# Kernel tuning notes

Measured on AMD Instinct MI355X. Metric: run time of the kernel, lower is better.

The kernel has to match this reference:

```python
import jax, jax.numpy as jnp
import numpy as np

N = 50000      # nodes
E = 800000     # edges (before self-loops)
F_IN = 128     # in_dim
H = 8          # heads
C = 16         # out_dim per head
NEG_SLOPE = 0.2
EPS = 1e-5


def setup_inputs() -> dict:
    key = jax.random.key(0)
    ks = jax.random.split(key, 8)
    x = jax.random.normal(ks[0], (N, F_IN), dtype=jnp.float32)
    edge_index = jax.random.randint(ks[1], (2, E), 0, N, dtype=jnp.int64)
    # GAT linear weight (xavier-ish scale), stored as [F_IN, H*C]
    W_gat = jax.random.normal(ks[2], (F_IN, H * C), dtype=jnp.float32) * 0.1
    att_src = jax.random.normal(ks[3], (H, C), dtype=jnp.float32) * 0.1
    att_dst = jax.random.normal(ks[4], (H, C), dtype=jnp.float32) * 0.1
    bias_gat = jnp.zeros((H * C,), dtype=jnp.float32)
    W_skip = jax.random.normal(ks[5], (F_IN, H * C), dtype=jnp.float32) * 0.1
    gamma = jnp.ones((H * C,), dtype=jnp.float32)
    beta = jnp.zeros((H * C,), dtype=jnp.float32)
    return {"x": x, "edge_index": edge_index, "W_gat": W_gat,
            "att_src": att_src, "att_dst": att_dst, "bias_gat": bias_gat,
            "W_skip": W_skip, "gamma": gamma, "beta": beta}


def reference(x, edge_index, W_gat, att_src, att_dst, bias_gat, W_skip, gamma, beta):
    # PyG GATConv default: add self-loops
    loop = jnp.arange(N, dtype=edge_index.dtype)
    src = jnp.concatenate([edge_index[0], loop])  # [E+N]
    dst = jnp.concatenate([edge_index[1], loop])  # [E+N]

    h = (x @ W_gat).reshape(N, H, C)              # [N,H,C]
    a_src = jnp.sum(h * att_src, axis=-1)          # [N,H]
    a_dst = jnp.sum(h * att_dst, axis=-1)          # [N,H]

    e = jax.nn.leaky_relu(a_src[src] + a_dst[dst], NEG_SLOPE)   # [E+N,H]
    # segment softmax over destination nodes
    e_max = jax.ops.segment_max(e, dst, num_segments=N)         # [N,H]
    e_exp = jnp.exp(e - e_max[dst])
    denom = jax.ops.segment_sum(e_exp, dst, num_segments=N)     # [N,H]
    alpha = e_exp / denom[dst]                                   # [E+N,H]

    msg = alpha[:, :, None] * h[src]                             # [E+N,H,C]
    gat_out = jax.ops.segment_sum(msg, dst, num_segments=N)     # [N,H,C]
    gat_out = gat_out.reshape(N, H * C) + bias_gat

    skip_out = x @ W_skip                                        # [N,H*C]
    z = gat_out + 0.1 * skip_out

    mu = jnp.mean(z, axis=-1, keepdims=True)
    var = jnp.mean((z - mu) ** 2, axis=-1, keepdims=True)
    z = (z - mu) * jax.lax.rsqrt(var + EPS) * gamma + beta
    return jax.nn.elu(z)  # dropout is identity in eval mode
```

## Files before the change

kernel.cpp:

```cpp
#include <hip/hip_runtime.h>
#include <hip/hip_bf16.h>

#define N_NODES 50000
#define N_EDGES 800000
#define F_IN    128
#define HC      128
#define NR      8
#define RSZ     6250
#define NCH     16
#define CHSZ    50000
#define NP      50048

typedef __attribute__((ext_vector_type(8))) short bf16x8;
typedef __attribute__((ext_vector_type(4))) float f32x4;

__device__ __forceinline__ float bf2f(unsigned int u16) {
    return __uint_as_float(u16 << 16);
}
__device__ __forceinline__ unsigned int f2bf(float f) {
    unsigned int u = __float_as_uint(f);
    return (u + 0x7fffu + ((u >> 16) & 1u)) >> 16;
}

__global__ __launch_bounds__(256) void k_hist(
    const int* __restrict__ dst,
    const float* __restrict__ Wg, const float* __restrict__ Ws,
    unsigned short* __restrict__ Bfrag, int* __restrict__ part)
{
    const int bid = blockIdx.x;
    const int tid = threadIdx.x;
    if (bid < 128) {
        __shared__ int hist[RSZ];
        const int r = bid & 7, c = bid >> 3;
        const int nb = r * RSZ;
        for (int i = tid; i < RSZ; i += 256) hist[i] = 0;
        __syncthreads();
        const int4* d4 = (const int4*)(dst + c * CHSZ);
        for (int i = tid; i < CHSZ / 4; i += 256) {
            const int4 v = d4[i];
            int b;
            b = v.x - nb; if ((unsigned)b < (unsigned)RSZ) atomicAdd(&hist[b], 1);
            b = v.y - nb; if ((unsigned)b < (unsigned)RSZ) atomicAdd(&hist[b], 1);
            b = v.z - nb; if ((unsigned)b < (unsigned)RSZ) atomicAdd(&hist[b], 1);
            b = v.w - nb; if ((unsigned)b < (unsigned)RSZ) atomicAdd(&hist[b], 1);
        }
        __syncthreads();
        for (int i = tid; i < RSZ; i += 256)
            part[(size_t)c * NP + nb + i] = hist[i];
    } else {
        const int g = (bid - 128) * 256 + tid;
        if (g < 4096) {
            const int lane = g & 63;
            const int kq = (g >> 6) & 3;
            const int nt = g >> 8;
            const int cc = nt * 16 + (lane & 15);
            const int kbase = kq * 32 + (lane >> 4) * 8;
            const float* Wsel = (cc < 128) ? (Wg + cc) : (Ws + cc - 128);
            unsigned int pk[4];
#pragma unroll
            for (int p = 0; p < 4; p++) {
                const float v0 = Wsel[(size_t)(kbase + 2 * p) * HC];
                const float v1 = Wsel[(size_t)(kbase + 2 * p + 1) * HC];
                pk[p] = f2bf(v0) | (f2bf(v1) << 16);
            }
            *(uint4*)(Bfrag + (size_t)g * 8) = make_uint4(pk[0], pk[1], pk[2], pk[3]);
        }
    }
}

__global__ __launch_bounds__(256) void k_scanA(
    int* __restrict__ part, int* __restrict__ counts,
    int* __restrict__ row_start, int* __restrict__ bsum)
{
    __shared__ int s[256];
    const int tid = threadIdx.x;
    const int base = blockIdx.x * 1024 + tid * 4;
    int v[4]; int t = 0;
#pragma unroll
    for (int j = 0; j < 4; j++) {
        const int idx = base + j;
        if (idx < N_NODES) {
            int run = 0;
#pragma unroll
            for (int c = 0; c < 16; c++) {
                int* p = part + (size_t)c * NP + idx;
                const int q = *p;
                *p = run;
                run += q;
            }
            counts[idx] = run;
            v[j] = run + 1;
        } else v[j] = 0;
        t += v[j];
    }
    s[tid] = t;
    __syncthreads();
    for (int off = 1; off < 256; off <<= 1) {
        int add = (tid >= off) ? s[tid - off] : 0;
        __syncthreads();
        s[tid] += add;
        __syncthreads();
    }
    int excl = s[tid] - t;
#pragma unroll
    for (int j = 0; j < 4; j++) {
        const int idx = base + j;
        if (idx < N_NODES) row_start[idx] = excl;
        excl += v[j];
    }
    if (tid == 255) bsum[blockIdx.x] = s[255];
}

__global__ void k_scanB(int* bsum, int nb) {
    int tid = threadIdx.x;
    int v = (tid < nb) ? bsum[tid] : 0;
    int orig = v;
    for (int off = 1; off < 64; off <<= 1) {
        int y = __shfl_up(v, off);
        if (tid >= off) v += y;
    }
    if (tid < nb) bsum[tid] = v - orig;
}

__global__ void k_scanC(int* __restrict__ row_start, const int* __restrict__ bsum,
                        const int* __restrict__ counts, int* __restrict__ csr) {
    int i = blockIdx.x * 256 + threadIdx.x;
    if (i < N_NODES) {
        int rs = row_start[i] + bsum[i >> 10];
        row_start[i] = rs;
        csr[rs + counts[i]] = i;
    }
}

__global__ __launch_bounds__(256) void k_lf(
    const float* __restrict__ x,
    const unsigned short* __restrict__ Bfrag,
    const float* __restrict__ att_s,
    const float* __restrict__ att_d,
    const float* __restrict__ bias,
    unsigned short* __restrict__ h_bf, unsigned int* __restrict__ z0b,
    float* __restrict__ a_src, float* __restrict__ a_dst,
    const int* __restrict__ src, const int* __restrict__ dst,
    const int* __restrict__ row_start, const int* __restrict__ part,
    int* __restrict__ csr)
{
    __shared__ __align__(16) int smem[RSZ];
    const int bid = blockIdx.x;
    const int tid = threadIdx.x;
    int lin = -1, r = 0, c = 0;
    if (bid < 256) {
        const int g = bid >> 4, pos = bid & 15;
        if (pos < 8) { r = pos; c = g; }
        else lin = g * 8 + (pos - 8);
    } else {
        lin = 128 + (bid - 256);
    }

    if (lin < 0) {
        const int nb = r * RSZ;
        for (int b = tid; b < RSZ; b += 256)
            smem[b] = row_start[nb + b] + part[(size_t)c * NP + nb + b];
        __syncthreads();
        const int4* d4 = (const int4*)(dst + c * CHSZ);
        const int4* s4 = (const int4*)(src + c * CHSZ);
        for (int i = tid; i < CHSZ / 4; i += 256) {
            const int4 dv = d4[i];
            const int4 sv = s4[i];
            int b;
            b = dv.x - nb; if ((unsigned)b < (unsigned)RSZ) csr[atomicAdd(&smem[b], 1)] = sv.x;
            b = dv.y - nb; if ((unsigned)b < (unsigned)RSZ) csr[atomicAdd(&smem[b], 1)] = sv.y;
            b = dv.z - nb; if ((unsigned)b < (unsigned)RSZ) csr[atomicAdd(&smem[b], 1)] = sv.z;
            b = dv.w - nb; if ((unsigned)b < (unsigned)RSZ) csr[atomicAdd(&smem[b], 1)] = sv.w;
        }
        return;
    }

    unsigned short* sA = (unsigned short*)smem;
    const int lane = tid & 63;
    const int w = tid >> 6;
    const int nbase = lin * 64;

#pragma unroll
    for (int it = 0; it < 4; it++) {
        const int p = it * 256 + tid;
        const int node = p >> 4;
        const int kg = p & 15;
        const int gn = nbase + node;
        float v[8];
        if (gn < N_NODES) {
            float4 u0 = *(const float4*)(x + (size_t)gn * F_IN + kg * 8);
            float4 u1 = *(const float4*)(x + (size_t)gn * F_IN + kg * 8 + 4);
            v[0] = u0.x; v[1] = u0.y; v[2] = u0.z; v[3] = u0.w;
            v[4] = u1.x; v[5] = u1.y; v[6] = u1.z; v[7] = u1.w;
        } else {
#pragma unroll
            for (int j = 0; j < 8; j++) v[j] = 0.f;
        }
        const int mt = node >> 4, lm = node & 15;
        const int kq = kg >> 2, quad = kg & 3;
        uint4 pk;
        pk.x = f2bf(v[0]) | (f2bf(v[1]) << 16);
        pk.y = f2bf(v[2]) | (f2bf(v[3]) << 16);
        pk.z = f2bf(v[4]) | (f2bf(v[5]) << 16);
        pk.w = f2bf(v[6]) | (f2bf(v[7]) << 16);
        *(uint4*)(sA + ((size_t)((mt * 4 + kq) * 64 + quad * 16 + lm)) * 8) = pk;
    }
    __syncthreads();

    const bf16x8* Bf = (const bf16x8*)Bfrag;
    f32x4 acc[4][4];
#pragma unroll
    for (int mt = 0; mt < 4; mt++)
#pragma unroll
        for (int nt = 0; nt < 4; nt++)
            acc[mt][nt] = (f32x4){0.f, 0.f, 0.f, 0.f};

#pragma unroll
    for (int kq = 0; kq < 4; kq++) {
        bf16x8 aF[4], bF[4];
#pragma unroll
        for (int nt = 0; nt < 4; nt++)
            bF[nt] = Bf[(size_t)(((w * 4 + nt) * 4 + kq) * 64 + lane)];
#pragma unroll
        for (int mt = 0; mt < 4; mt++)
            aF[mt] = *(const bf16x8*)(sA + ((size_t)((mt * 4 + kq) * 64 + lane)) * 8);
#pragma unroll
        for (int mt = 0; mt < 4; mt++)
#pragma unroll
            for (int nt = 0; nt < 4; nt++)
                acc[mt][nt] = __builtin_amdgcn_mfma_f32_16x16x32_bf16(
                    aF[mt], bF[nt], acc[mt][nt], 0, 0, 0);
    }

    const int row4 = (lane >> 4) * 4;
    const int cl = lane & 15;
#pragma unroll
    for (int mt = 0; mt < 4; mt++) {
#pragma unroll
        for (int nt = 0; nt < 4; nt++) {
            const int cc = w * 64 + nt * 16 + cl;
            f32x4 d = acc[mt][nt];
            if (cc < 128) {
                const float asv = att_s[cc];
                const float adv = att_d[cc];
                float ps[4], pd[4];
#pragma unroll
                for (int rr = 0; rr < 4; rr++) { ps[rr] = d[rr] * asv; pd[rr] = d[rr] * adv; }
#pragma unroll
                for (int m = 1; m <= 8; m <<= 1) {
#pragma unroll
                    for (int rr = 0; rr < 4; rr++) {
                        ps[rr] += __shfl_xor(ps[rr], m);
                        pd[rr] += __shfl_xor(pd[rr], m);
                    }
                }
                const int head = w * 4 + nt;
#pragma unroll
                for (int rr = 0; rr < 4; rr++) {
                    const int gn = nbase + mt * 16 + row4 + rr;
                    if (gn < N_NODES) {
                        h_bf[(size_t)gn * HC + cc] = (unsigned short)f2bf(d[rr]);
                        if (cl == 0) {
                            a_src[gn * 8 + head] = ps[rr];
                            a_dst[gn * 8 + head] = pd[rr];
                        }
                    }
                }
            } else {
                const int cz = cc - 128;
                const float bv = bias[cz];
#pragma unroll
                for (int rr = 0; rr < 4; rr++) {
                    const int gn = nbase + mt * 16 + row4 + rr;
                    const float val = 0.1f * d[rr] + bv;
                    const float oth = __shfl_xor(val, 1);
                    if ((cl & 1) == 0 && gn < N_NODES) {
                        z0b[(size_t)gn * 64 + (cz >> 1)] =
                            f2bf(val) | (f2bf(oth) << 16);
                    }
                }
            }
        }
    }
}

__global__ __launch_bounds__(256) void k_agg(
    const uint2* __restrict__ h2,
    const uint2* __restrict__ z0b,
    const float* __restrict__ a_src, const float* __restrict__ a_dst,
    const int* __restrict__ row_start, const int* __restrict__ counts,
    const int* __restrict__ csr,
    const float* __restrict__ gamma, const float* __restrict__ beta,
    float* __restrict__ out)
{
    const int tid = threadIdx.x;
    const int lane = tid & 63;
    const int l = lane & 31;
    const int n = blockIdx.x * 8 + ((tid >> 6) << 1) + (lane >> 5);
    const int head = l >> 2;

    const float adn = a_dst[n * 8 + head];
    const int rs = row_start[n];
    const int cnt = counts[n] + 1;

    float d_acc = 0.f, a0 = 0.f, a1 = 0.f, a2 = 0.f, a3 = 0.f;
    for (int i = 0; i < cnt; i += 8) {
        int s[8]; float ae[8], mk[8]; uint2 hp[8];
#pragma unroll
        for (int j = 0; j < 8; j++) {
            const int e = i + j;
            const int ec = (e < cnt) ? e : (cnt - 1);
            mk[j] = (e < cnt) ? 1.f : 0.f;
            s[j] = csr[rs + ec];
        }
#pragma unroll
        for (int j = 0; j < 8; j++) ae[j] = a_src[s[j] * 8 + head];
#pragma unroll
        for (int j = 0; j < 8; j++) hp[j] = h2[(size_t)s[j] * 32 + l];
#pragma unroll
        for (int j = 0; j < 8; j++) {
            float e = ae[j] + adn;
            e = (e > 0.f) ? e : 0.2f * e;
            const float wgt = __expf(e) * mk[j];
            d_acc += wgt;
            a0 += wgt * bf2f(hp[j].x & 0xffffu);
            a1 += wgt * bf2f(hp[j].x >> 16);
            a2 += wgt * bf2f(hp[j].y & 0xffffu);
            a3 += wgt * bf2f(hp[j].y >> 16);
        }
    }
    const float inv = 1.0f / d_acc;
    const uint2 zp = z0b[(size_t)n * 32 + l];
    float y0 = a0 * inv + bf2f(zp.x & 0xffffu);
    float y1 = a1 * inv + bf2f(zp.x >> 16);
    float y2 = a2 * inv + bf2f(zp.y & 0xffffu);
    float y3 = a3 * inv + bf2f(zp.y >> 16);

    float ss = y0 + y1 + y2 + y3;
#pragma unroll
    for (int off = 1; off < 32; off <<= 1) ss += __shfl_xor(ss, off);
    const float mu = ss * (1.0f / 128.0f);
    const float d0 = y0 - mu, d1 = y1 - mu, d2 = y2 - mu, d3 = y3 - mu;
    float vs = d0 * d0 + d1 * d1 + d2 * d2 + d3 * d3;
#pragma unroll
    for (int off = 1; off < 32; off <<= 1) vs += __shfl_xor(vs, off);
    const float rstd = rsqrtf(vs * (1.0f / 128.0f) + 1e-5f);

    const float4 gv = *(const float4*)(gamma + l * 4);
    const float4 bv = *(const float4*)(beta + l * 4);
    float o0 = d0 * rstd * gv.x + bv.x;
    float o1 = d1 * rstd * gv.y + bv.y;
    float o2 = d2 * rstd * gv.z + bv.z;
    float o3 = d3 * rstd * gv.w + bv.w;
    o0 = (o0 > 0.f) ? o0 : (__expf(o0) - 1.0f);
    o1 = (o1 > 0.f) ? o1 : (__expf(o1) - 1.0f);
    o2 = (o2 > 0.f) ? o2 : (__expf(o2) - 1.0f);
    o3 = (o3 > 0.f) ? o3 : (__expf(o3) - 1.0f);

    *(float4*)(out + (size_t)n * HC + l * 4) = make_float4(o0, o1, o2, o3);
}

extern "C" void kernel_launch(void* const* d_in, const int* in_sizes, int n_in,
                              void* d_out, int out_size, void* d_ws, size_t ws_size,
                              hipStream_t stream) {
    const float* x   = (const float*)d_in[0];
    const int*   ei  = (const int*)d_in[1];
    const float* Wg  = (const float*)d_in[2];
    const float* as_ = (const float*)d_in[3];
    const float* ad_ = (const float*)d_in[4];
    const float* bg  = (const float*)d_in[5];
    const float* Wsk = (const float*)d_in[6];
    const float* gm  = (const float*)d_in[7];
    const float* bt  = (const float*)d_in[8];
    float* out = (float*)d_out;

    char* wsb = (char*)d_ws;
    unsigned short* h_bf  = (unsigned short*)wsb;
    unsigned int*   z0b   = (unsigned int*)(wsb + 12800000);
    float*          a_src = (float*)(wsb + 25600000);
    float*          a_dst = (float*)(wsb + 27200000);
    unsigned short* Bfrag = (unsigned short*)(wsb + 28800000);
    int*   counts = (int*)(wsb + 28865536);
    int*   row_st = (int*)(wsb + 29065728);
    int*   bsum   = (int*)(wsb + 29265920);
    int*   csr    = (int*)(wsb + 29266944);
    int*   part   = (int*)(wsb + 32666944);

    const int* src = ei;
    const int* dst = ei + N_EDGES;

    k_hist <<<144, 256, 0, stream>>>(dst, Wg, Wsk, Bfrag, part);
    k_scanA<<<49, 256, 0, stream>>>(part, counts, row_st, bsum);
    k_scanB<<<1, 64, 0, stream>>>(bsum, 49);
    k_scanC<<<196, 256, 0, stream>>>(row_st, bsum, counts, csr);
    k_lf   <<<910, 256, 0, stream>>>(x, Bfrag, as_, ad_, bg, h_bf, z0b,
                                     a_src, a_dst, src, dst, row_st, part, csr);
    k_agg  <<<N_NODES / 8, 256, 0, stream>>>((const uint2*)h_bf, (const uint2*)z0b,
                                             a_src, a_dst, row_st, counts, csr,
                                             gm, bt, out);
}
```

Measured before the change: 210.4 us.

## Fold block-sum scan into scanC, stage h in LDS, use one wave per node

The separate single-block scan of block sums is removed; each scanC block computes its own prefix offset with a wave reduction, which drops one kernel launch. In k_lf the bf16 h tile is staged through shared memory so it can be written out as coalesced 16-byte stores, and the attention dot products are computed from the staged rows instead of through per-fragment shuffle reductions. k_agg now assigns a full 64-lane wave to each node, with each lane holding two channels instead of four. This gives more parallelism and more in-flight gathers per edge, but issues more instructions per edge and doubles the wave count.

```diff
diff --git a/kernel.cpp b/kernel.cpp
--- a/kernel.cpp
+++ b/kernel.cpp
@@ -111,22 +111,23 @@
     if (tid == 255) bsum[blockIdx.x] = s[255];
 }
 
-__global__ void k_scanB(int* bsum, int nb) {
-    int tid = threadIdx.x;
-    int v = (tid < nb) ? bsum[tid] : 0;
-    int orig = v;
-    for (int off = 1; off < 64; off <<= 1) {
-        int y = __shfl_up(v, off);
-        if (tid >= off) v += y;
-    }
-    if (tid < nb) bsum[tid] = v - orig;
-}
-
-__global__ void k_scanC(int* __restrict__ row_start, const int* __restrict__ bsum,
-                        const int* __restrict__ counts, int* __restrict__ csr) {
-    int i = blockIdx.x * 256 + threadIdx.x;
+__global__ __launch_bounds__(256) void k_scanC(
+    int* __restrict__ row_start, const int* __restrict__ bsum,
+    const int* __restrict__ counts, int* __restrict__ csr)
+{
+    __shared__ int soff;
+    const int tid = threadIdx.x;
+    if (tid < 64) {
+        const int tgt = blockIdx.x >> 2;
+        int v = (tid < 49 && tid < tgt) ? bsum[tid] : 0;
+#pragma unroll
+        for (int off = 1; off < 64; off <<= 1) v += __shfl_xor(v, off);
+        if (tid == 0) soff = v;
+    }
+    __syncthreads();
+    const int i = blockIdx.x * 256 + tid;
     if (i < N_NODES) {
-        int rs = row_start[i] + bsum[i >> 10];
+        const int rs = row_start[i] + soff;
         row_start[i] = rs;
         csr[rs + counts[i]] = i;
     }
@@ -232,61 +233,93 @@
                     aF[mt], bF[nt], acc[mt][nt], 0, 0, 0);
     }
 
+    __syncthreads();
+
     const int row4 = (lane >> 4) * 4;
     const int cl = lane & 15;
-#pragma unroll
-    for (int mt = 0; mt < 4; mt++) {
-#pragma unroll
-        for (int nt = 0; nt < 4; nt++) {
-            const int cc = w * 64 + nt * 16 + cl;
-            f32x4 d = acc[mt][nt];
-            if (cc < 128) {
-                const float asv = att_s[cc];
-                const float adv = att_d[cc];
-                float ps[4], pd[4];
-#pragma unroll
-                for (int rr = 0; rr < 4; rr++) { ps[rr] = d[rr] * asv; pd[rr] = d[rr] * adv; }
-#pragma unroll
-                for (int m = 1; m <= 8; m <<= 1) {
-#pragma unroll
-                    for (int rr = 0; rr < 4; rr++) {
-                        ps[rr] += __shfl_xor(ps[rr], m);
-                        pd[rr] += __shfl_xor(pd[rr], m);
+    unsigned int* hls = (unsigned int*)smem;
+
+    if (w < 2) {
+#pragma unroll
+        for (int mt = 0; mt < 4; mt++) {
+#pragma unroll
+            for (int nt = 0; nt < 4; nt++) {
+                const int cc = w * 64 + nt * 16 + cl;
+                f32x4 d = acc[mt][nt];
+#pragma unroll
+                for (int rr = 0; rr < 4; rr++) {
+                    const float oth = __shfl_xor(d[rr], 1);
+                    if ((cl & 1) == 0) {
+                        const int nl = mt * 16 + row4 + rr;
+                        hls[nl * 68 + (cc >> 1)] = f2bf(d[rr]) | (f2bf(oth) << 16);
                     }
                 }
-                const int head = w * 4 + nt;
-#pragma unroll
-                for (int rr = 0; rr < 4; rr++) {
-                    const int gn = nbase + mt * 16 + row4 + rr;
-                    if (gn < N_NODES) {
-                        h_bf[(size_t)gn * HC + cc] = (unsigned short)f2bf(d[rr]);
-                        if (cl == 0) {
-                            a_src[gn * 8 + head] = ps[rr];
-                            a_dst[gn * 8 + head] = pd[rr];
-                        }
-                    }
-                }
-            } else {
-                const int cz = cc - 128;
+            }
+        }
+    } else {
+#pragma unroll
+        for (int mt = 0; mt < 4; mt++) {
+#pragma unroll
+            for (int nt = 0; nt < 4; nt++) {
+                const int cz = (w - 2) * 64 + nt * 16 + cl;
+                f32x4 d = acc[mt][nt];
                 const float bv = bias[cz];
 #pragma unroll
                 for (int rr = 0; rr < 4; rr++) {
                     const int gn = nbase + mt * 16 + row4 + rr;
                     const float val = 0.1f * d[rr] + bv;
                     const float oth = __shfl_xor(val, 1);
-                    if ((cl & 1) == 0 && gn < N_NODES) {
-                        z0b[(size_t)gn * 64 + (cz >> 1)] =
-                            f2bf(val) | (f2bf(oth) << 16);
-                    }
+                    if ((cl & 1) == 0 && gn < N_NODES)
+                        z0b[(size_t)gn * 64 + (cz >> 1)] = f2bf(val) | (f2bf(oth) << 16);
                 }
             }
         }
     }
+    __syncthreads();
+
+    {
+        const int row = tid >> 2, q = tid & 3;
+        const int gn = nbase + row;
+        if (gn < N_NODES) {
+            const unsigned int* hr = hls + row * 68 + q * 16;
+            uint4 v0 = *(const uint4*)(hr);
+            uint4 v1 = *(const uint4*)(hr + 4);
+            uint4 v2 = *(const uint4*)(hr + 8);
+            uint4 v3 = *(const uint4*)(hr + 12);
+            uint4* hout = (uint4*)((unsigned int*)h_bf + (size_t)gn * 64 + q * 16);
+            hout[0] = v0; hout[1] = v1; hout[2] = v2; hout[3] = v3;
+
+            const unsigned int u[16] = {v0.x, v0.y, v0.z, v0.w,
+                                        v1.x, v1.y, v1.z, v1.w,
+                                        v2.x, v2.y, v2.z, v2.w,
+                                        v3.x, v3.y, v3.z, v3.w};
+            const int c0 = q * 32;
+            const float4* as4 = (const float4*)(att_s + c0);
+            const float4* ad4 = (const float4*)(att_d + c0);
+            float ds0 = 0.f, dd0 = 0.f, ds1 = 0.f, dd1 = 0.f;
+#pragma unroll
+            for (int j = 0; j < 4; j++) {
+                const float4 sa = as4[j], da = ad4[j];
+                float l0 = bf2f(u[2 * j] & 0xffffu),     h0v = bf2f(u[2 * j] >> 16);
+                float l1 = bf2f(u[2 * j + 1] & 0xffffu), h1v = bf2f(u[2 * j + 1] >> 16);
+                ds0 += l0 * sa.x + h0v * sa.y + l1 * sa.z + h1v * sa.w;
+                dd0 += l0 * da.x + h0v * da.y + l1 * da.z + h1v * da.w;
+                const float4 sb = as4[4 + j], db = ad4[4 + j];
+                float l2 = bf2f(u[8 + 2 * j] & 0xffffu),     h2v = bf2f(u[8 + 2 * j] >> 16);
+                float l3 = bf2f(u[8 + 2 * j + 1] & 0xffffu), h3v = bf2f(u[8 + 2 * j + 1] >> 16);
+                ds1 += l2 * sb.x + h2v * sb.y + l3 * sb.z + h3v * sb.w;
+                dd1 += l2 * db.x + h2v * db.y + l3 * db.z + h3v * db.w;
+            }
+            const int hh = 2 * q;
+            a_src[gn * 8 + hh] = ds0;     a_src[gn * 8 + hh + 1] = ds1;
+            a_dst[gn * 8 + hh] = dd0;     a_dst[gn * 8 + hh + 1] = dd1;
+        }
+    }
 }
 
 __global__ __launch_bounds__(256) void k_agg(
-    const uint2* __restrict__ h2,
-    const uint2* __restrict__ z0b,
+    const unsigned int* __restrict__ h32,
+    const unsigned int* __restrict__ z0b,
     const float* __restrict__ a_src, const float* __restrict__ a_dst,
     const int* __restrict__ row_start, const int* __restrict__ counts,
     const int* __restrict__ csr,
@@ -295,17 +328,16 @@
 {
     const int tid = threadIdx.x;
     const int lane = tid & 63;
-    const int l = lane & 31;
-    const int n = blockIdx.x * 8 + ((tid >> 6) << 1) + (lane >> 5);
-    const int head = l >> 2;
+    const int n = blockIdx.x * 4 + (tid >> 6);
+    const int head = lane >> 3;
 
     const float adn = a_dst[n * 8 + head];
-    const int rs = row_start[n];
-    const int cnt = counts[n] + 1;
-
-    float d_acc = 0.f, a0 = 0.f, a1 = 0.f, a2 = 0.f, a3 = 0.f;
+    const int rs  = __builtin_amdgcn_readfirstlane(row_start[n]);
+    const int cnt = __builtin_amdgcn_readfirstlane(counts[n]) + 1;
+
+    float d_acc = 0.f, a0 = 0.f, a1 = 0.f;
     for (int i = 0; i < cnt; i += 8) {
-        int s[8]; float ae[8], mk[8]; uint2 hp[8];
+        int s[8]; float ae[8], mk[8]; unsigned int hp[8];
 #pragma unroll
         for (int j = 0; j < 8; j++) {
             const int e = i + j;
@@ -316,48 +348,40 @@
 #pragma unroll
         for (int j = 0; j < 8; j++) ae[j] = a_src[s[j] * 8 + head];
 #pragma unroll
-        for (int j = 0; j < 8; j++) hp[j] = h2[(size_t)s[j] * 32 + l];
+        for (int j = 0; j < 8; j++) hp[j] = h32[(size_t)s[j] * 64 + lane];
 #pragma unroll
         for (int j = 0; j < 8; j++) {
             float e = ae[j] + adn;
             e = (e > 0.f) ? e : 0.2f * e;
             const float wgt = __expf(e) * mk[j];
             d_acc += wgt;
-            a0 += wgt * bf2f(hp[j].x & 0xffffu);
-            a1 += wgt * bf2f(hp[j].x >> 16);
-            a2 += wgt * bf2f(hp[j].y & 0xffffu);
-            a3 += wgt * bf2f(hp[j].y >> 16);
+            a0 += wgt * bf2f(hp[j] & 0xffffu);
+            a1 += wgt * bf2f(hp[j] >> 16);
         }
     }
     const float inv = 1.0f / d_acc;
-    const uint2 zp = z0b[(size_t)n * 32 + l];
-    float y0 = a0 * inv + bf2f(zp.x & 0xffffu);
-    float y1 = a1 * inv + bf2f(zp.x >> 16);
-    float y2 = a2 * inv + bf2f(zp.y & 0xffffu);
-    float y3 = a3 * inv + bf2f(zp.y >> 16);
-
-    float ss = y0 + y1 + y2 + y3;
-#pragma unroll
-    for (int off = 1; off < 32; off <<= 1) ss += __shfl_xor(ss, off);
+    const unsigned int zp = z0b[(size_t)n * 64 + lane];
+    float y0 = a0 * inv + bf2f(zp & 0xffffu);
+    float y1 = a1 * inv + bf2f(zp >> 16);
+
+    float ss = y0 + y1;
+#pragma unroll
+    for (int off = 1; off < 64; off <<= 1) ss += __shfl_xor(ss, off);
     const float mu = ss * (1.0f / 128.0f);
-    const float d0 = y0 - mu, d1 = y1 - mu, d2 = y2 - mu, d3 = y3 - mu;
-    float vs = d0 * d0 + d1 * d1 + d2 * d2 + d3 * d3;
-#pragma unroll
-    for (int off = 1; off < 32; off <<= 1) vs += __shfl_xor(vs, off);
+    const float d0 = y0 - mu, d1 = y1 - mu;
+    float vs = d0 * d0 + d1 * d1;
+#pragma unroll
+    for (int off = 1; off < 64; off <<= 1) vs += __shfl_xor(vs, off);
     const float rstd = rsqrtf(vs * (1.0f / 128.0f) + 1e-5f);
 
-    const float4 gv = *(const float4*)(gamma + l * 4);
-    const float4 bv = *(const float4*)(beta + l * 4);
+    const float2 gv = *(const float2*)(gamma + lane * 2);
+    const float2 bv = *(const float2*)(beta + lane * 2);
     float o0 = d0 * rstd * gv.x + bv.x;
     float o1 = d1 * rstd * gv.y + bv.y;
-    float o2 = d2 * rstd * gv.z + bv.z;
-    float o3 = d3 * rstd * gv.w + bv.w;
     o0 = (o0 > 0.f) ? o0 : (__expf(o0) - 1.0f);
     o1 = (o1 > 0.f) ? o1 : (__expf(o1) - 1.0f);
-    o2 = (o2 > 0.f) ? o2 : (__expf(o2) - 1.0f);
-    o3 = (o3 > 0.f) ? o3 : (__expf(o3) - 1.0f);
-
-    *(float4*)(out + (size_t)n * HC + l * 4) = make_float4(o0, o1, o2, o3);
+
+    *(float2*)(out + (size_t)n * HC + lane * 2) = make_float2(o0, o1);
 }
 
 extern "C" void kernel_launch(void* const* d_in, const int* in_sizes, int n_in,
@@ -391,11 +415,10 @@
 
     k_hist <<<144, 256, 0, stream>>>(dst, Wg, Wsk, Bfrag, part);
     k_scanA<<<49, 256, 0, stream>>>(part, counts, row_st, bsum);
-    k_scanB<<<1, 64, 0, stream>>>(bsum, 49);
     k_scanC<<<196, 256, 0, stream>>>(row_st, bsum, counts, csr);
     k_lf   <<<910, 256, 0, stream>>>(x, Bfrag, as_, ad_, bg, h_bf, z0b,
                                      a_src, a_dst, src, dst, row_st, part, csr);
-    k_agg  <<<N_NODES / 8, 256, 0, stream>>>((const uint2*)h_bf, (const uint2*)z0b,
+    k_agg  <<<N_NODES / 4, 256, 0, stream>>>((const unsigned int*)h_bf, z0b,
                                              a_src, a_dst, row_st, counts, csr,
                                              gm, bt, out);
 }
```

New measurement: 213.1 us. Within noise of the previous version (+1.3%).
